# Performance work log

Measured on AMD Instinct MI355X. Metric: run time of the kernel, lower is better.

Reference implementation:

```python
import jax, jax.numpy as jnp
import numpy as np

B, S, HID = 2, 2048, 2048
H, KVH, D = 16, 4, 128
GROUPS = H // KVH  # 4


def apply_rotary(x, cos, sin):
    # x: [B, h, S, D]; cos/sin: [S, D//2]
    xr = x[..., 0::2]
    xi = x[..., 1::2]
    c = cos[None, None, :, :]
    s = sin[None, None, :, :]
    orr = xr * c - xi * s
    oi = xr * s + xi * c
    return jnp.stack([orr, oi], axis=-1).reshape(x.shape)


def setup_inputs() -> dict:
    key = jax.random.key(0)
    k0, k1, k2, k3, k4 = jax.random.split(key, 5)
    x = jax.random.normal(k0, (B, S, HID), dtype=jnp.float32)
    # real RoPE frequencies (llama-style), stored as [S, D//2, 2] = (cos, sin)
    inv_freq = 1.0 / (10000.0 ** (np.arange(0, D, 2, dtype=np.float32) / D))
    t = np.arange(S, dtype=np.float32)
    ang = np.outer(t, inv_freq)  # [S, D//2]
    freqs_cis = jnp.asarray(np.stack([np.cos(ang), np.sin(ang)], axis=-1), dtype=jnp.float32)
    sc = 0.02
    wq = jax.random.normal(k1, (HID, H * D), dtype=jnp.float32) * sc
    wk = jax.random.normal(k2, (HID, KVH * D), dtype=jnp.float32) * sc
    wv = jax.random.normal(k3, (HID, KVH * D), dtype=jnp.float32) * sc
    wo = jax.random.normal(k4, (H * D, HID), dtype=jnp.float32) * sc
    return {"x": x, "freqs_cis": freqs_cis, "wq": wq, "wk": wk, "wv": wv, "wo": wo}


def reference(x, freqs_cis, wq, wk, wv, wo):
    b, s, _ = x.shape
    cos, sin = freqs_cis[..., 0], freqs_cis[..., 1]
    q = (x @ wq).reshape(b, s, H, D).transpose(0, 2, 1, 3)    # [B,H,S,D]
    k = (x @ wk).reshape(b, s, KVH, D).transpose(0, 2, 1, 3)  # [B,KVH,S,D]
    v = (x @ wv).reshape(b, s, KVH, D).transpose(0, 2, 1, 3)
    q = apply_rotary(q, cos, sin)
    k = apply_rotary(k, cos, sin)
    # GQA expand: repeat kv heads into query-head groups
    k = jnp.repeat(k, GROUPS, axis=1)  # [B,H,S,D]
    v = jnp.repeat(v, GROUPS, axis=1)
    scale = 1.0 / jnp.sqrt(jnp.asarray(D, dtype=x.dtype))
    scores = jnp.einsum("bhqd,bhkd->bhqk", q, k) * scale
    causal = jnp.tril(jnp.ones((s, s), dtype=bool))
    scores = jnp.where(causal[None, None], scores, jnp.asarray(-jnp.inf, dtype=scores.dtype))
    attn = jax.nn.softmax(scores, axis=-1)
    out = jnp.einsum("bhqk,bhkd->bhqd", attn, v)
    out = out.transpose(0, 2, 1, 3).reshape(b, s, H * D)
    return out @ wo
```

## Files before the change

### kernel.cpp

```cpp
#include <hip/hip_runtime.h>
#include <hip/hip_bf16.h>

#define B_   2
#define S_   2048
#define HID_ 2048
#define H_   16
#define KVH_ 4
#define D_   128
#define M_   4096
#define NQKV 3072

typedef __attribute__((ext_vector_type(8))) short bf16x8;
typedef __attribute__((ext_vector_type(4))) float f32x4;
typedef const __attribute__((address_space(1))) unsigned int* gas_p;
typedef __attribute__((address_space(3))) unsigned int* las_p;

__device__ __forceinline__ unsigned short f2b(float f) {
    __hip_bfloat16 h = __float2bfloat16(f);
    return *reinterpret_cast<unsigned short*>(&h);
}
__device__ __forceinline__ float b2f(unsigned short u) {
    __hip_bfloat16 h;
    *reinterpret_cast<unsigned short*>(&h) = u;
    return __bfloat162float(h);
}

__global__ __launch_bounds__(256)
void convert_x(const float* __restrict__ x, unsigned short* __restrict__ xb) {
    int i = (blockIdx.x * 256 + threadIdx.x) * 4;
    float4 v = *(const float4*)(x + i);
    ushort4 o;
    o.x = f2b(v.x); o.y = f2b(v.y); o.z = f2b(v.z); o.w = f2b(v.w);
    *(ushort4*)(xb + i) = o;
}

__global__ __launch_bounds__(256)
void convert_w_all(const float* __restrict__ wq, const float* __restrict__ wk,
                   const float* __restrict__ wv, const float* __restrict__ wo,
                   unsigned short* __restrict__ wqkvT,
                   unsigned short* __restrict__ woT) {
    __shared__ float tile[32][33];
    int z = blockIdx.z;
    const float* w; int N, nbase; unsigned short* dst;
    if (z == 0)      { w = wq; N = 2048; nbase = 0;    dst = wqkvT; }
    else if (z == 1) { w = wk; N = 512;  nbase = 2048; dst = wqkvT; }
    else if (z == 2) { w = wv; N = 512;  nbase = 2560; dst = wqkvT; }
    else             { w = wo; N = 2048; nbase = 0;    dst = woT; }
    int n0 = blockIdx.x * 32, k0 = blockIdx.y * 32;
    if (n0 >= N) return;
    int tx = threadIdx.x & 31, ty = threadIdx.x >> 5;
    #pragma unroll
    for (int j = 0; j < 4; j++)
        tile[ty + j*8][tx] = w[(size_t)(k0 + ty + j*8) * N + n0 + tx];
    __syncthreads();
    #pragma unroll
    for (int j = 0; j < 4; j++)
        dst[(size_t)(nbase + n0 + ty + j*8) * 2048 + k0 + tx] = f2b(tile[tx][ty + j*8]);
}

#define BAR    asm volatile("s_barrier" ::: "memory")
#define LG0    do { asm volatile("s_waitcnt lgkmcnt(0)" ::: "memory"); \
                    __builtin_amdgcn_sched_barrier(0); } while (0)
#define GATE0  asm volatile("s_waitcnt vmcnt(0)" ::: "memory")
#define GATE6  asm volatile("s_waitcnt vmcnt(6)" ::: "memory")
#define GATE8  asm volatile("s_waitcnt vmcnt(8)" ::: "memory")
#define PHI    __builtin_amdgcn_s_setprio(1)
#define PLO    __builtin_amdgcn_s_setprio(0)

#define STG(srcrow, ldsbase, half, tile) do {                                   \
    _Pragma("unroll")                                                           \
    for (int it_ = 0; it_ < 2; ++it_) {                                         \
      int p_ = w * 128 + it_ * 64 + lane;                                       \
      int r_ = (half) * 128 + (p_ >> 3);                                        \
      int q8_ = ((p_ & 7) ^ ((p_ >> 3) & 7)) * 8;                               \
      __builtin_amdgcn_global_load_lds(                                         \
          (gas_p)((srcrow) + (size_t)r_ * 2048 + (tile) * 64 + q8_),            \
          (las_p)((char*)(ldsbase) + ((half) * 1024 + w * 128 + it_ * 64) * 16),\
          16, 0, 0);                                                            \
    } } while (0)

#define RDA2(dst, bufi, mi) do {                                                \
    const unsigned short* Ab_ = &As[bufi][0] + (mi)*8192 + wr*4096 + l15*64;    \
    _Pragma("unroll")                                                           \
    for (int f_ = 0; f_ < 4; ++f_) {                                            \
      dst[f_][0] = *(const bf16x8*)(Ab_ + f_*1024 + slot0);                     \
      dst[f_][1] = *(const bf16x8*)(Ab_ + f_*1024 + slot1);                     \
    } } while (0)

#define RDB2(dst, bufi, ni) do {                                                \
    const unsigned short* Bb_ = &Bs[bufi][0] + (ni)*8192 + wc*2048 + l15*64;    \
    _Pragma("unroll")                                                           \
    for (int g_ = 0; g_ < 2; ++g_) {                                            \
      dst[g_][0] = *(const bf16x8*)(Bb_ + g_*1024 + slot0);                     \
      dst[g_][1] = *(const bf16x8*)(Bb_ + g_*1024 + slot1);                     \
    } } while (0)

#define MMQ(ra, rb, mi, ni) do {                                                \
    _Pragma("unroll")                                                           \
    for (int f_ = 0; f_ < 4; ++f_)                                              \
      _Pragma("unroll")                                                         \
      for (int g_ = 0; g_ < 2; ++g_) {                                          \
        acc[(mi)*4+f_][(ni)*2+g_] = __builtin_amdgcn_mfma_f32_16x16x32_bf16(    \
            ra[f_][0], rb[g_][0], acc[(mi)*4+f_][(ni)*2+g_], 0, 0, 0);          \
        acc[(mi)*4+f_][(ni)*2+g_] = __builtin_amdgcn_mfma_f32_16x16x32_bf16(    \
            ra[f_][1], rb[g_][1], acc[(mi)*4+f_][(ni)*2+g_], 0, 0, 0);          \
      } } while (0)

__global__ __launch_bounds__(512)
void gemm8(const unsigned short* __restrict__ A,
           const unsigned short* __restrict__ BT,
           unsigned short* __restrict__ qkvb,
           unsigned short* __restrict__ vTb,
           const float* __restrict__ freqs) {
    __shared__ unsigned short As[2][16384];
    __shared__ unsigned short Bs[2][16384];

    int tid  = threadIdx.x;
    int lane = tid & 63, w = tid >> 6;
    int l15  = lane & 15, quad = lane >> 4;
    int wr = w >> 2, wc = w & 3;
    int bid = blockIdx.y * 12 + blockIdx.x;
    int s_  = (bid & 7) * 24 + (bid >> 3);
    int by  = s_ / 12, bx = s_ % 12;
    int row0 = by * 256, col0 = bx * 256;
    int slot0 = (quad ^ (lane & 7)) * 8;
    int slot1 = slot0 ^ 32;

    const unsigned short* Arow = A  + (size_t)row0 * 2048;
    const unsigned short* Brow = BT + (size_t)col0 * 2048;

    f32x4 acc[8][4];
    #pragma unroll
    for (int i = 0; i < 8; ++i)
        #pragma unroll
        for (int j = 0; j < 4; ++j) acc[i][j] = f32x4{0.f, 0.f, 0.f, 0.f};

    bf16x8 ra0[4][2], ra1[4][2];
    bf16x8 rb0[2][2], rb1[2][2];

    STG(Brow, &Bs[0][0], 0, 0);
    STG(Arow, &As[0][0], 0, 0);
    STG(Arow, &As[0][0], 1, 0);
    STG(Brow, &Bs[0][0], 1, 0);
    STG(Brow, &Bs[1][0], 0, 1);
    STG(Arow, &As[1][0], 0, 1);
    STG(Arow, &As[1][0], 1, 1);
    STG(Brow, &Bs[1][0], 1, 1);
    GATE8;
    BAR;
    RDB2(rb0, 0, 0);
    RDA2(ra0, 0, 0);

    #pragma unroll 1
    for (int i = 0; i < 16; ++i) {
        int t  = 2 * i;
        int t2 = (t + 2 > 31) ? 31 : t + 2;
        int t3 = (t + 3 > 31) ? 31 : t + 3;
        RDA2(ra1, 0, 1);
        STG(Brow, &Bs[0][0], 0, t2);
        PHI; MMQ(ra0, rb0, 0, 0); PLO;
        BAR;
        RDB2(rb1, 0, 1);
        STG(Arow, &As[0][0], 0, t2);
        PHI; MMQ(ra1, rb0, 1, 0); PLO;
        GATE8; BAR;
        RDB2(rb0, 1, 0);
        STG(Arow, &As[0][0], 1, t2);
        PHI; MMQ(ra0, rb1, 0, 1); PLO;
        BAR;
        RDA2(ra0, 1, 0);
        STG(Brow, &Bs[0][0], 1, t2);
        PHI; MMQ(ra1, rb1, 1, 1); PLO;
        GATE8; BAR;
        RDA2(ra1, 1, 1);
        STG(Brow, &Bs[1][0], 0, t3);
        PHI; MMQ(ra0, rb0, 0, 0); PLO;
        BAR;
        RDB2(rb1, 1, 1);
        STG(Arow, &As[1][0], 0, t3);
        PHI; MMQ(ra1, rb0, 1, 0); PLO;
        GATE8; BAR;
        RDB2(rb0, 0, 0);
        STG(Arow, &As[1][0], 1, t3);
        PHI; MMQ(ra0, rb1, 0, 1); PLO;
        BAR;
        RDA2(ra0, 0, 0);
        STG(Brow, &Bs[1][0], 1, t3);
        PHI; MMQ(ra1, rb1, 1, 1); PLO;
        GATE8; BAR;
    }

    int q4 = quad * 4;
    if (col0 < 2560) {
        const float qscale = 0.08838834764831845f;
        #pragma unroll
        for (int mi = 0; mi < 2; ++mi)
        #pragma unroll
        for (int f = 0; f < 4; ++f) {
            int mb = row0 + mi*128 + wr*64 + f*16 + q4;
            #pragma unroll
            for (int ni = 0; ni < 2; ++ni)
            #pragma unroll
            for (int g = 0; g < 2; ++g) {
                int colb = col0 + ni*128 + wc*32 + g*16 + l15;
                int dd = (colb & 127) & ~1;
                bool odd = colb & 1;
                float sc = (colb < 2048) ? qscale : 1.f;
                #pragma unroll
                for (int rr = 0; rr < 4; ++rr) {
                    int m = mb + rr;
                    int s = m & 2047;
                    float v  = acc[mi*4 + f][ni*2 + g][rr];
                    float pv = __shfl_xor(v, 1);
                    float cs = freqs[s*128 + dd];
                    float sn = freqs[s*128 + dd + 1];
                    float o  = odd ? (pv*sn + v*cs) : (v*cs - pv*sn);
                    qkvb[(size_t)m * NQKV + colb] = f2b(o * sc);
                }
            }
        }
    } else {
        #pragma unroll
        for (int mi = 0; mi < 2; ++mi)
        #pragma unroll
        for (int f = 0; f < 4; ++f) {
            int mb = row0 + mi*128 + wr*64 + f*16 + q4;
            int s0 = mb & 2047;
            #pragma unroll
            for (int ni = 0; ni < 2; ++ni)
            #pragma unroll
            for (int g = 0; g < 2; ++g) {
                int colb = col0 + ni*128 + wc*32 + g*16 + l15;
                int vrow = (row0 >> 11) * 512 + (colb - 2560);
                ushort4 ov;
                ov.x = f2b(acc[mi*4 + f][ni*2 + g][0]);
                ov.y = f2b(acc[mi*4 + f][ni*2 + g][1]);
                ov.z = f2b(acc[mi*4 + f][ni*2 + g][2]);
                ov.w = f2b(acc[mi*4 + f][ni*2 + g][3]);
                *(ushort4*)(vTb + (size_t)vrow * 2048 + s0) = ov;
            }
        }
    }
}

#define RDAo(bufi) do {                                                         \
    const unsigned short* Ab_ = &As[bufi][0] + wr * 4096 + l15 * 64;            \
    _Pragma("unroll")                                                           \
    for (int f_ = 0; f_ < 4; ++f_) {                                            \
      af[f_][0] = *(const bf16x8*)(Ab_ + f_ * 1024 + slot0);                    \
      af[f_][1] = *(const bf16x8*)(Ab_ + f_ * 1024 + slot1);                    \
    } } while (0)

#define RDBo(bufi, g) do {                                                      \
    const unsigned short* Bb_ = &Bs[bufi][0] + wc * 4096 + l15 * 64;            \
    bfr[g][0] = *(const bf16x8*)(Bb_ + (g) * 1024 + slot0);                     \
    bfr[g][1] = *(const bf16x8*)(Bb_ + (g) * 1024 + slot1);                     \
    } while (0)

#define MM8o(mi, ni) do {                                                       \
    _Pragma("unroll")                                                           \
    for (int f_ = 2*(mi); f_ < 2*(mi)+2; ++f_)                                  \
      _Pragma("unroll")                                                         \
      for (int g_ = 2*(ni); g_ < 2*(ni)+2; ++g_) {                              \
        acc[f_][g_] = __builtin_amdgcn_mfma_f32_16x16x32_bf16(                  \
            af[f_][0], bfr[g_][0], acc[f_][g_], 0, 0, 0);                       \
        acc[f_][g_] = __builtin_amdgcn_mfma_f32_16x16x32_bf16(                  \
            af[f_][1], bfr[g_][1], acc[f_][g_], 0, 0, 0);                       \
      } } while (0)

__global__ __launch_bounds__(512)
void gemm8o(const unsigned short* __restrict__ A,
            const unsigned short* __restrict__ BT,
            float* __restrict__ Cf) {
    __shared__ unsigned short As[2][16384];
    __shared__ unsigned short Bs[2][8192];

    int tid  = threadIdx.x;
    int lane = tid & 63, w = tid >> 6;
    int l15  = lane & 15, quad = lane >> 4;
    int wr = w >> 1, wc = w & 1;
    int bid = blockIdx.y * 16 + blockIdx.x;
    int s_  = (bid & 7) * 32 + (bid >> 3);
    int by  = s_ >> 4, bx = s_ & 15;
    int row0 = by * 256, col0 = bx * 128;
    int slot0 = (quad ^ (lane & 7)) * 8;
    int slot1 = slot0 ^ 32;

    const unsigned short* Arow = A  + (size_t)row0 * 2048;
    const unsigned short* Brow = BT + (size_t)col0 * 2048;

    f32x4 acc[4][4];
    #pragma unroll
    for (int i = 0; i < 4; ++i)
        #pragma unroll
        for (int j = 0; j < 4; ++j) acc[i][j] = f32x4{0.f, 0.f, 0.f, 0.f};

    bf16x8 af[4][2];
    bf16x8 bfr[4][2];

    STG(Arow, &As[0][0], 0, 0);
    STG(Arow, &As[0][0], 1, 0);
    STG(Brow, &Bs[0][0], 0, 0);
    STG(Arow, &As[1][0], 0, 1);
    STG(Arow, &As[1][0], 1, 1);
    STG(Brow, &Bs[1][0], 0, 1);
    GATE6;
    BAR;

    #pragma unroll 1
    for (int i = 0; i < 15; ++i) {
        int t = 2 * i;
        RDAo(0); RDBo(0, 0); RDBo(0, 1);
        BAR; LG0; PHI; MM8o(0, 0); PLO; BAR;
        RDBo(0, 2); RDBo(0, 3); STG(Arow, &As[0][0], 0, t + 2);
        BAR; LG0; PHI; MM8o(0, 1); PLO; BAR;
        STG(Arow, &As[0][0], 1, t + 2);
        BAR; LG0; PHI; MM8o(1, 0); PLO; BAR;
        STG(Brow, &Bs[0][0], 0, t + 2);
        BAR; LG0; PHI; MM8o(1, 1); PLO; GATE6; BAR;
        RDAo(1); RDBo(1, 0); RDBo(1, 1);
        BAR; LG0; PHI; MM8o(0, 0); PLO; BAR;
        RDBo(1, 2); RDBo(1, 3); STG(Arow, &As[1][0], 0, t + 3);
        BAR; LG0; PHI; MM8o(0, 1); PLO; BAR;
        STG(Arow, &As[1][0], 1, t + 3);
        BAR; LG0; PHI; MM8o(1, 0); PLO; BAR;
        STG(Brow, &Bs[1][0], 0, t + 3);
        BAR; LG0; PHI; MM8o(1, 1); PLO; GATE6; BAR;
    }
    RDAo(0); RDBo(0, 0); RDBo(0, 1);
    BAR; LG0; PHI; MM8o(0, 0); PLO; BAR;
    RDBo(0, 2); RDBo(0, 3);
    BAR; LG0; PHI; MM8o(0, 1); PLO; BAR;
    BAR; LG0; PHI; MM8o(1, 0); PLO; BAR;
    BAR; LG0; PHI; MM8o(1, 1); PLO; GATE0; BAR;
    RDAo(1); RDBo(1, 0); RDBo(1, 1);
    BAR; LG0; PHI; MM8o(0, 0); PLO; BAR;
    RDBo(1, 2); RDBo(1, 3);
    BAR; LG0; PHI; MM8o(0, 1); PLO; BAR;
    BAR; LG0; PHI; MM8o(1, 0); PLO; BAR;
    LG0; PHI; MM8o(1, 1); PLO;

    int q4 = quad * 4;
    #pragma unroll
    for (int f = 0; f < 4; ++f) {
        int mb = row0 + wr*64 + f*16 + q4;
        #pragma unroll
        for (int g = 0; g < 4; ++g) {
            int colb = col0 + wc*64 + g*16 + l15;
            #pragma unroll
            for (int rr = 0; rr < 4; ++rr)
                Cf[(size_t)(mb + rr) * 2048 + colb] = acc[f][g][rr];
        }
    }
}

__global__ __launch_bounds__(512)
void attn_mfma(const unsigned short* __restrict__ qkv,
               const unsigned short* __restrict__ vT,
               unsigned short* __restrict__ ao,
               unsigned short* __restrict__ wsP,
               float2* __restrict__ wsML) {
    __shared__ unsigned short Ks[64 * 128];
    __shared__ unsigned short Vt[128 * 64];

    int tid  = threadIdx.x;
    int lane = tid & 63, w = tid >> 6;
    int quad = lane >> 4, l15 = lane & 15;
    int hw = w >> 1, qhalf = w & 1;
    int bx = blockIdx.x, hk = blockIdx.y, b = blockIdx.z;
    int h = hk * 4 + hw;

    int qt, c;
    if (bx < 12)      { qt = 31 - bx / 3;        c = bx % 3; }
    else if (bx < 40) { qt = 27 - (bx - 12) / 2; c = (bx - 12) & 1; }
    else              { qt = 53 - bx;            c = 0; }
    int nt = qt + 1;
    int nch = (qt >= 28) ? 3 : (qt >= 14 ? 2 : 1);
    int kt_begin = c * 14;
    int kt_end = (nt < (c + 1) * 14) ? nt : (c + 1) * 14;
    bool lastc = (c == nch - 1);
    int q0 = qt * 64;

    bf16x8 aq[2][4];
    #pragma unroll
    for (int qf = 0; qf < 2; qf++) {
        const unsigned short* qrow =
            qkv + (size_t)(b*2048 + q0 + qhalf*32 + qf*16 + l15) * NQKV + h*128;
        #pragma unroll
        for (int k4 = 0; k4 < 4; k4++)
            aq[qf][k4] = *(const bf16x8*)(qrow + k4*32 + quad*8);
    }

    int koff[4][4];
    #pragma unroll
    for (int j = 0; j < 4; j++) {
        int row = ((j >> 1) * 32) + ((l15 >> 2) * 8) + ((j & 1) * 4) + (l15 & 3);
        #pragma unroll
        for (int k4 = 0; k4 < 4; k4++) {
            int slot = (k4 * 4 + quad) ^ (row & 15);
            koff[j][k4] = (row * 16 + slot) * 8;
        }
    }
    int vbase0 = (l15 * 8 + (quad ^ (l15 & 7))) * 8;
    int vbase1 = (l15 * 8 + ((4 + quad) ^ (l15 & 7))) * 8;

    const unsigned short* kb0 = qkv + (size_t)(b*2048) * NQKV + 2048 + hk*128;
    const unsigned short* vb0 = vT + (size_t)(b*512 + hk*128) * 2048;

    auto stage_k = [&](int kt) {
        #pragma unroll
        for (int it = 0; it < 2; it++) {
            int s = w * 128 + it * 64 + lane;
            int r = s >> 4, qp = s & 15;
            int q = qp ^ (r & 15);
            __builtin_amdgcn_global_load_lds(
                (gas_p)(kb0 + (size_t)(kt*64 + r) * NQKV + q * 8),
                (las_p)((char*)&Ks[0] + (w * 128 + it * 64) * 16),
                16, 0, 0);
        }
    };
    auto stage_v = [&](int kt) {
        #pragma unroll
        for (int it = 0; it < 2; it++) {
            int s = w * 128 + it * 64 + lane;
            int r = s >> 3, qp = s & 7;
            int q = qp ^ (r & 7);
            __builtin_amdgcn_global_load_lds(
                (gas_p)(vb0 + (size_t)r * 2048 + kt*64 + q * 8),
                (las_p)((char*)&Vt[0] + (w * 128 + it * 64) * 16),
                16, 0, 0);
        }
    };

    f32x4 o_acc[2][8];
    const f32x4 zf = {0.f, 0.f, 0.f, 0.f};
    #pragma unroll
    for (int qf = 0; qf < 2; qf++)
        #pragma unroll
        for (int jn = 0; jn < 8; jn++) o_acc[qf][jn] = zf;
    float m_i[2] = {-1e30f, -1e30f}, l_i[2] = {0.f, 0.f};
    int qglob[2] = {q0 + qhalf*32 + l15, q0 + qhalf*32 + 16 + l15};

    stage_k(kt_begin);
    for (int kt = kt_begin; kt < kt_end; kt++) {
        __syncthreads();
        stage_v(kt);

        f32x4 s_acc[2][4];
        #pragma unroll
        for (int j = 0; j < 4; j++) {
            s_acc[0][j] = zf; s_acc[1][j] = zf;
            #pragma unroll
            for (int k4 = 0; k4 < 4; k4++) {
                bf16x8 ak = *(const bf16x8*)&Ks[koff[j][k4]];
                s_acc[0][j] = __builtin_amdgcn_mfma_f32_16x16x32_bf16(ak, aq[0][k4], s_acc[0][j], 0, 0, 0);
                s_acc[1][j] = __builtin_amdgcn_mfma_f32_16x16x32_bf16(ak, aq[1][k4], s_acc[1][j], 0, 0, 0);
            }
        }

        bf16x8 pp[2][2];
        #pragma unroll
        for (int qf = 0; qf < 2; qf++) {
            float sv[4][4];
            #pragma unroll
            for (int j = 0; j < 4; j++)
                #pragma unroll
                for (int r = 0; r < 4; r++)
                    sv[j][r] = s_acc[qf][j][r];
            if (kt == qt) {
                #pragma unroll
                for (int j = 0; j < 4; j++)
                    #pragma unroll
                    for (int r = 0; r < 4; r++) {
                        int sloc = ((j >> 1) * 32) + quad*8 + ((j & 1) * 4) + r;
                        if (kt*64 + sloc > qglob[qf]) sv[j][r] = -1e30f;
                    }
            }
            float mx = sv[0][0];
            #pragma unroll
            for (int j = 0; j < 4; j++)
                #pragma unroll
                for (int r = 0; r < 4; r++) mx = fmaxf(mx, sv[j][r]);
            mx = fmaxf(mx, __shfl_xor(mx, 16));
            mx = fmaxf(mx, __shfl_xor(mx, 32));
            int defer = __all(mx <= m_i[qf] + 8.f);
            float mnew = defer ? m_i[qf] : fmaxf(m_i[qf], mx);
            float rs = 0.f;
            float p[4][4];
            #pragma unroll
            for (int j = 0; j < 4; j++)
                #pragma unroll
                for (int r = 0; r < 4; r++) {
                    p[j][r] = __expf(sv[j][r] - mnew);
                    rs += p[j][r];
                }
            if (!defer) {
                float alpha = __expf(m_i[qf] - mnew);
                l_i[qf] *= alpha;
                #pragma unroll
                for (int jn = 0; jn < 8; jn++)
                    #pragma unroll
                    for (int r = 0; r < 4; r++) o_acc[qf][jn][r] *= alpha;
                m_i[qf] = mnew;
            }
            l_i[qf] += rs;
            #pragma unroll
            for (int r = 0; r < 4; r++) {
                pp[qf][0][r]     = (short)f2b(p[0][r]);
                pp[qf][0][r + 4] = (short)f2b(p[1][r]);
                pp[qf][1][r]     = (short)f2b(p[2][r]);
                pp[qf][1][r + 4] = (short)f2b(p[3][r]);
            }
        }

        __syncthreads();
        if (kt + 1 < kt_end) stage_k(kt + 1);

        #pragma unroll
        for (int jn = 0; jn < 8; jn++) {
            bf16x8 av0 = *(const bf16x8*)&Vt[jn*1024 + vbase0];
            bf16x8 av1 = *(const bf16x8*)&Vt[jn*1024 + vbase1];
            o_acc[0][jn] = __builtin_amdgcn_mfma_f32_16x16x32_bf16(av0, pp[0][0], o_acc[0][jn], 0, 0, 0);
            o_acc[0][jn] = __builtin_amdgcn_mfma_f32_16x16x32_bf16(av1, pp[0][1], o_acc[0][jn], 0, 0, 0);
            o_acc[1][jn] = __builtin_amdgcn_mfma_f32_16x16x32_bf16(av0, pp[1][0], o_acc[1][jn], 0, 0, 0);
            o_acc[1][jn] = __builtin_amdgcn_mfma_f32_16x16x32_bf16(av1, pp[1][1], o_acc[1][jn], 0, 0, 0);
        }
    }

    int pi = 0, mi = 0;
    if (qt >= 14) {
        if (qt < 28) { mi = (qt - 14) * 2 + c;       pi = qt - 14; }
        else         { mi = 28 + (qt - 28) * 3 + c;  pi = 14 + (qt - 28) * 2 + c; }
    }
    #pragma unroll
    for (int qf = 0; qf < 2; qf++) {
        float lt = l_i[qf];
        lt += __shfl_xor(lt, 16);
        lt += __shfl_xor(lt, 32);
        float inv = 1.f / lt;
        int q_local = qhalf * 32 + qf * 16 + l15;
        unsigned short* dst;
        if (lastc)
            dst = ao + (size_t)(b*2048 + q0 + q_local) * 2048 + h*128;
        else
            dst = wsP + (size_t)(((pi * 8 + hk * 2 + b) * 4 + hw) * 64 + q_local) * 128;
        #pragma unroll
        for (int jn = 0; jn < 8; jn++) {
            ushort4 ov;
            ov.x = f2b(o_acc[qf][jn][0] * inv);
            ov.y = f2b(o_acc[qf][jn][1] * inv);
            ov.z = f2b(o_acc[qf][jn][2] * inv);
            ov.w = f2b(o_acc[qf][jn][3] * inv);
            *(ushort4*)(dst + jn*16 + quad*4) = ov;
        }
        if (qt >= 14 && quad == 0)
            wsML[(mi * 8 + hk * 2 + b) * 256 + hw * 64 + q_local]
                = make_float2(m_i[qf], lt);
    }
}

__global__ __launch_bounds__(256)
void merge_kernel(unsigned short* __restrict__ ao,
                  const unsigned short* __restrict__ wsP,
                  const float2* __restrict__ wsML) {
    int t = blockIdx.x * 256 + threadIdx.x;
    int d = (t & 15) * 8;
    int h = (t >> 4) & 15;
    int rest = t >> 8;
    int q_off = rest % 1152;
    int b = rest / 1152;
    int q = 896 + q_off;
    int qt = q >> 6, q_local = q & 63;
    int hk = h >> 2, hw = h & 3;
    int nch = (qt >= 28) ? 3 : 2;

    float mv[3], lv[3];
    for (int cc = 0; cc < nch; cc++) {
        int mi = (qt < 28) ? (qt - 14) * 2 + cc : 28 + (qt - 28) * 3 + cc;
        float2 ml = wsML[(mi * 8 + hk * 2 + b) * 256 + hw * 64 + q_local];
        mv[cc] = ml.x; lv[cc] = ml.y;
    }
    float M = mv[0];
    for (int cc = 1; cc < nch; cc++) M = fmaxf(M, mv[cc]);
    float f[3], S = 0.f;
    for (int cc = 0; cc < nch; cc++) { f[cc] = __expf(mv[cc] - M) * lv[cc]; S += f[cc]; }
    float inv = 1.f / S;

    unsigned short* arow = ao + (size_t)(b*2048 + q) * 2048 + h*128 + d;
    float outv[8];
    {
        ushort4 a0 = *(ushort4*)arow, a1 = *(ushort4*)(arow + 4);
        float fl = f[nch-1];
        outv[0] = fl*b2f(a0.x); outv[1] = fl*b2f(a0.y);
        outv[2] = fl*b2f(a0.z); outv[3] = fl*b2f(a0.w);
        outv[4] = fl*b2f(a1.x); outv[5] = fl*b2f(a1.y);
        outv[6] = fl*b2f(a1.z); outv[7] = fl*b2f(a1.w);
    }
    for (int cc = 0; cc < nch - 1; cc++) {
        int pi = (qt < 28) ? (qt - 14) : 14 + (qt - 28) * 2 + cc;
        const unsigned short* prow =
            wsP + (size_t)(((pi * 8 + hk * 2 + b) * 4 + hw) * 64 + q_local) * 128 + d;
        ushort4 p0 = *(const ushort4*)prow, p1 = *(const ushort4*)(prow + 4);
        float fc = f[cc];
        outv[0] += fc*b2f(p0.x); outv[1] += fc*b2f(p0.y);
        outv[2] += fc*b2f(p0.z); outv[3] += fc*b2f(p0.w);
        outv[4] += fc*b2f(p1.x); outv[5] += fc*b2f(p1.y);
        outv[6] += fc*b2f(p1.z); outv[7] += fc*b2f(p1.w);
    }
    ushort4 o0, o1;
    o0.x = f2b(outv[0]*inv); o0.y = f2b(outv[1]*inv);
    o0.z = f2b(outv[2]*inv); o0.w = f2b(outv[3]*inv);
    o1.x = f2b(outv[4]*inv); o1.y = f2b(outv[5]*inv);
    o1.z = f2b(outv[6]*inv); o1.w = f2b(outv[7]*inv);
    *(ushort4*)arow = o0;
    *(ushort4*)(arow + 4) = o1;
}

extern "C" void kernel_launch(void* const* d_in, const int* in_sizes, int n_in,
                              void* d_out, int out_size, void* d_ws, size_t ws_size,
                              hipStream_t stream) {
    const float* x     = (const float*)d_in[0];
    const float* freqs = (const float*)d_in[1];
    const float* wq    = (const float*)d_in[2];
    const float* wk    = (const float*)d_in[3];
    const float* wv    = (const float*)d_in[4];
    const float* wo    = (const float*)d_in[5];
    float* out = (float*)d_out;

    char* ws = (char*)d_ws;
    unsigned short* xbf    = (unsigned short*)(ws);
    unsigned short* aobuf  = (unsigned short*)(ws);
    unsigned short* wqkvT  = (unsigned short*)(ws + (16u<<20));
    unsigned short* woT    = (unsigned short*)(ws + (28u<<20));
    unsigned short* qkvbuf = (unsigned short*)(ws + (36u<<20));
    unsigned short* vTbuf  = (unsigned short*)(ws + (60u<<20));
    unsigned short* wsP  = (unsigned short*)(ws + (16u<<20));
    float2*         wsML = (float2*)(ws + (16u<<20) + 176u*65536u);

    dim3 blk(256);
    convert_x<<<8192, blk, 0, stream>>>(x, xbf);
    convert_w_all<<<dim3(64, 64, 4), blk, 0, stream>>>(wq, wk, wv, wo, wqkvT, woT);
    gemm8<<<dim3(NQKV/256, M_/256), dim3(512), 0, stream>>>(
        xbf, wqkvT, qkvbuf, vTbuf, freqs);
    attn_mfma<<<dim3(54, 4, 2), dim3(512), 0, stream>>>(qkvbuf, vTbuf, aobuf, wsP, wsML);
    merge_kernel<<<2304, blk, 0, stream>>>(aobuf, wsP, wsML);
    gemm8o<<<dim3(2048/128, M_/256), dim3(512), 0, stream>>>(aobuf, woT, out);
}
```

Before: 319.3 us.

## Retile QKV GEMM to 256x192 tiles and merge conversion kernels

The QKV projection GEMM moves from 256x256 tiles on a 12x16 grid to 256x192 tiles on a 16x16 grid. This gives 256 workgroups, matching the CU count better and removing the partial last wave. The warp layout changes from 2x4 to 4x2 and the main loop is restructured with finer barrier and lgkmcnt gating plus a peeled epilogue. The Q/K/V epilogue branch becomes per-column-group because a tile now straddles regions. The x and weight conversion kernels are fused into one launch to save a kernel launch, at the cost of more barriers per K step in the GEMM.

```diff
diff --git a/kernel.cpp b/kernel.cpp
--- a/kernel.cpp
+++ b/kernel.cpp
@@ -26,21 +26,23 @@
 }
 
 __global__ __launch_bounds__(256)
-void convert_x(const float* __restrict__ x, unsigned short* __restrict__ xb) {
-    int i = (blockIdx.x * 256 + threadIdx.x) * 4;
-    float4 v = *(const float4*)(x + i);
-    ushort4 o;
-    o.x = f2b(v.x); o.y = f2b(v.y); o.z = f2b(v.z); o.w = f2b(v.w);
-    *(ushort4*)(xb + i) = o;
-}
-
-__global__ __launch_bounds__(256)
-void convert_w_all(const float* __restrict__ wq, const float* __restrict__ wk,
-                   const float* __restrict__ wv, const float* __restrict__ wo,
-                   unsigned short* __restrict__ wqkvT,
-                   unsigned short* __restrict__ woT) {
+void convert_all(const float* __restrict__ x,
+                 const float* __restrict__ wq, const float* __restrict__ wk,
+                 const float* __restrict__ wv, const float* __restrict__ wo,
+                 unsigned short* __restrict__ xb,
+                 unsigned short* __restrict__ wqkvT,
+                 unsigned short* __restrict__ woT) {
+    int z = blockIdx.z;
+    if (z >= 4) {
+        int lin = ((z - 4) * 64 + blockIdx.y) * 64 + blockIdx.x;
+        int i = (lin * 256 + threadIdx.x) * 4;
+        float4 v = *(const float4*)(x + i);
+        ushort4 o;
+        o.x = f2b(v.x); o.y = f2b(v.y); o.z = f2b(v.z); o.w = f2b(v.w);
+        *(ushort4*)(xb + i) = o;
+        return;
+    }
     __shared__ float tile[32][33];
-    int z = blockIdx.z;
     const float* w; int N, nbase; unsigned short* dst;
     if (z == 0)      { w = wq; N = 2048; nbase = 0;    dst = wqkvT; }
     else if (z == 1) { w = wk; N = 512;  nbase = 2048; dst = wqkvT; }
@@ -63,7 +65,7 @@
                     __builtin_amdgcn_sched_barrier(0); } while (0)
 #define GATE0  asm volatile("s_waitcnt vmcnt(0)" ::: "memory")
 #define GATE6  asm volatile("s_waitcnt vmcnt(6)" ::: "memory")
-#define GATE8  asm volatile("s_waitcnt vmcnt(8)" ::: "memory")
+#define GATE7  asm volatile("s_waitcnt vmcnt(7)" ::: "memory")
 #define PHI    __builtin_amdgcn_s_setprio(1)
 #define PLO    __builtin_amdgcn_s_setprio(0)
 
@@ -79,31 +81,41 @@
           16, 0, 0);                                                            \
     } } while (0)
 
-#define RDA2(dst, bufi, mi) do {                                                \
-    const unsigned short* Ab_ = &As[bufi][0] + (mi)*8192 + wr*4096 + l15*64;    \
+#define STGB(srcrow, ldsbase, unit, tile) do {                                  \
+      int p_ = w * 64 + lane;                                                   \
+      int r_ = (unit) * 64 + (p_ >> 3);                                         \
+      int q8_ = ((p_ & 7) ^ ((p_ >> 3) & 7)) * 8;                               \
+      __builtin_amdgcn_global_load_lds(                                         \
+          (gas_p)((srcrow) + (size_t)r_ * 2048 + (tile) * 64 + q8_),            \
+          (las_p)((char*)(ldsbase) + ((unit) * 512 + p_) * 16),                 \
+          16, 0, 0);                                                            \
+    } while (0)
+
+#define RDAq(dst, bufi) do {                                                    \
+    const unsigned short* Ab_ = &As[bufi][0] + wr*4096 + l15*64;                \
     _Pragma("unroll")                                                           \
     for (int f_ = 0; f_ < 4; ++f_) {                                            \
       dst[f_][0] = *(const bf16x8*)(Ab_ + f_*1024 + slot0);                     \
       dst[f_][1] = *(const bf16x8*)(Ab_ + f_*1024 + slot1);                     \
     } } while (0)
 
-#define RDB2(dst, bufi, ni) do {                                                \
-    const unsigned short* Bb_ = &Bs[bufi][0] + (ni)*8192 + wc*2048 + l15*64;    \
+#define RDBq(dst, bufi, nh) do {                                                \
+    const unsigned short* Bb_ = &Bs[bufi][0] + wc*6144 + (nh)*3072 + l15*64;    \
     _Pragma("unroll")                                                           \
-    for (int g_ = 0; g_ < 2; ++g_) {                                            \
+    for (int g_ = 0; g_ < 3; ++g_) {                                            \
       dst[g_][0] = *(const bf16x8*)(Bb_ + g_*1024 + slot0);                     \
       dst[g_][1] = *(const bf16x8*)(Bb_ + g_*1024 + slot1);                     \
     } } while (0)
 
-#define MMQ(ra, rb, mi, ni) do {                                                \
+#define MMq(mh, rb, nh) do {                                                    \
     _Pragma("unroll")                                                           \
-    for (int f_ = 0; f_ < 4; ++f_)                                              \
+    for (int f_ = 2*(mh); f_ < 2*(mh)+2; ++f_)                                  \
       _Pragma("unroll")                                                         \
-      for (int g_ = 0; g_ < 2; ++g_) {                                          \
-        acc[(mi)*4+f_][(ni)*2+g_] = __builtin_amdgcn_mfma_f32_16x16x32_bf16(    \
-            ra[f_][0], rb[g_][0], acc[(mi)*4+f_][(ni)*2+g_], 0, 0, 0);          \
-        acc[(mi)*4+f_][(ni)*2+g_] = __builtin_amdgcn_mfma_f32_16x16x32_bf16(    \
-            ra[f_][1], rb[g_][1], acc[(mi)*4+f_][(ni)*2+g_], 0, 0, 0);          \
+      for (int g_ = 0; g_ < 3; ++g_) {                                          \
+        acc[f_][(nh)*3+g_] = __builtin_amdgcn_mfma_f32_16x16x32_bf16(           \
+            ra[f_][0], rb[g_][0], acc[f_][(nh)*3+g_], 0, 0, 0);                 \
+        acc[f_][(nh)*3+g_] = __builtin_amdgcn_mfma_f32_16x16x32_bf16(           \
+            ra[f_][1], rb[g_][1], acc[f_][(nh)*3+g_], 0, 0, 0);                 \
       } } while (0)
 
 __global__ __launch_bounds__(512)
@@ -113,130 +125,114 @@
            unsigned short* __restrict__ vTb,
            const float* __restrict__ freqs) {
     __shared__ unsigned short As[2][16384];
-    __shared__ unsigned short Bs[2][16384];
+    __shared__ unsigned short Bs[2][12288];
 
     int tid  = threadIdx.x;
     int lane = tid & 63, w = tid >> 6;
     int l15  = lane & 15, quad = lane >> 4;
-    int wr = w >> 2, wc = w & 3;
-    int bid = blockIdx.y * 12 + blockIdx.x;
-    int s_  = (bid & 7) * 24 + (bid >> 3);
-    int by  = s_ / 12, bx = s_ % 12;
-    int row0 = by * 256, col0 = bx * 256;
+    int wr = w >> 1, wc = w & 1;
+    int bid = blockIdx.y * 16 + blockIdx.x;
+    int s_  = (bid & 7) * 32 + (bid >> 3);
+    int by  = s_ >> 4, bx = s_ & 15;
+    int row0 = by * 256, col0 = bx * 192;
     int slot0 = (quad ^ (lane & 7)) * 8;
     int slot1 = slot0 ^ 32;
 
     const unsigned short* Arow = A  + (size_t)row0 * 2048;
     const unsigned short* Brow = BT + (size_t)col0 * 2048;
 
-    f32x4 acc[8][4];
-    #pragma unroll
-    for (int i = 0; i < 8; ++i)
-        #pragma unroll
-        for (int j = 0; j < 4; ++j) acc[i][j] = f32x4{0.f, 0.f, 0.f, 0.f};
-
-    bf16x8 ra0[4][2], ra1[4][2];
-    bf16x8 rb0[2][2], rb1[2][2];
-
-    STG(Brow, &Bs[0][0], 0, 0);
-    STG(Arow, &As[0][0], 0, 0);
-    STG(Arow, &As[0][0], 1, 0);
-    STG(Brow, &Bs[0][0], 1, 0);
-    STG(Brow, &Bs[1][0], 0, 1);
-    STG(Arow, &As[1][0], 0, 1);
-    STG(Arow, &As[1][0], 1, 1);
-    STG(Brow, &Bs[1][0], 1, 1);
-    GATE8;
+    f32x4 acc[4][6];
+    #pragma unroll
+    for (int i = 0; i < 4; ++i)
+        #pragma unroll
+        for (int j = 0; j < 6; ++j) acc[i][j] = f32x4{0.f, 0.f, 0.f, 0.f};
+
+    bf16x8 ra[4][2];
+    bf16x8 rbl[3][2];
+    bf16x8 rbh[3][2];
+
+    STG (Arow, &As[0][0], 0, 0);
+    STG (Arow, &As[0][0], 1, 0);
+    STGB(Brow, &Bs[0][0], 0, 0);
+    STGB(Brow, &Bs[0][0], 1, 0);
+    STGB(Brow, &Bs[0][0], 2, 0);
+    STG (Arow, &As[1][0], 0, 1);
+    STG (Arow, &As[1][0], 1, 1);
+    STGB(Brow, &Bs[1][0], 0, 1);
+    STGB(Brow, &Bs[1][0], 1, 1);
+    STGB(Brow, &Bs[1][0], 2, 1);
+    GATE7;
     BAR;
-    RDB2(rb0, 0, 0);
-    RDA2(ra0, 0, 0);
 
     #pragma unroll 1
-    for (int i = 0; i < 16; ++i) {
-        int t  = 2 * i;
-        int t2 = (t + 2 > 31) ? 31 : t + 2;
-        int t3 = (t + 3 > 31) ? 31 : t + 3;
-        RDA2(ra1, 0, 1);
-        STG(Brow, &Bs[0][0], 0, t2);
-        PHI; MMQ(ra0, rb0, 0, 0); PLO;
-        BAR;
-        RDB2(rb1, 0, 1);
-        STG(Arow, &As[0][0], 0, t2);
-        PHI; MMQ(ra1, rb0, 1, 0); PLO;
-        GATE8; BAR;
-        RDB2(rb0, 1, 0);
-        STG(Arow, &As[0][0], 1, t2);
-        PHI; MMQ(ra0, rb1, 0, 1); PLO;
-        BAR;
-        RDA2(ra0, 1, 0);
-        STG(Brow, &Bs[0][0], 1, t2);
-        PHI; MMQ(ra1, rb1, 1, 1); PLO;
-        GATE8; BAR;
-        RDA2(ra1, 1, 1);
-        STG(Brow, &Bs[1][0], 0, t3);
-        PHI; MMQ(ra0, rb0, 0, 0); PLO;
-        BAR;
-        RDB2(rb1, 1, 1);
-        STG(Arow, &As[1][0], 0, t3);
-        PHI; MMQ(ra1, rb0, 1, 0); PLO;
-        GATE8; BAR;
-        RDB2(rb0, 0, 0);
-        STG(Arow, &As[1][0], 1, t3);
-        PHI; MMQ(ra0, rb1, 0, 1); PLO;
-        BAR;
-        RDA2(ra0, 0, 0);
-        STG(Brow, &Bs[1][0], 1, t3);
-        PHI; MMQ(ra1, rb1, 1, 1); PLO;
-        GATE8; BAR;
-    }
+    for (int i = 0; i < 15; ++i) {
+        int t = 2 * i;
+        RDAq(ra, 0); RDBq(rbl, 0, 0);
+        BAR; LG0; PHI; MMq(0, rbl, 0); PLO; BAR;
+        RDBq(rbh, 0, 1); STG(Arow, &As[0][0], 0, t + 2);
+        BAR; LG0; PHI; MMq(0, rbh, 1); PLO; BAR;
+        STG(Arow, &As[0][0], 1, t + 2);
+        BAR; LG0; PHI; MMq(1, rbl, 0); PLO; BAR;
+        STGB(Brow, &Bs[0][0], 0, t + 2);
+        STGB(Brow, &Bs[0][0], 1, t + 2);
+        STGB(Brow, &Bs[0][0], 2, t + 2);
+        BAR; LG0; PHI; MMq(1, rbh, 1); PLO; GATE7; BAR;
+        RDAq(ra, 1); RDBq(rbl, 1, 0);
+        BAR; LG0; PHI; MMq(0, rbl, 0); PLO; BAR;
+        RDBq(rbh, 1, 1); STG(Arow, &As[1][0], 0, t + 3);
+        BAR; LG0; PHI; MMq(0, rbh, 1); PLO; BAR;
+        STG(Arow, &As[1][0], 1, t + 3);
+        BAR; LG0; PHI; MMq(1, rbl, 0); PLO; BAR;
+        STGB(Brow, &Bs[1][0], 0, t + 3);
+        STGB(Brow, &Bs[1][0], 1, t + 3);
+        STGB(Brow, &Bs[1][0], 2, t + 3);
+        BAR; LG0; PHI; MMq(1, rbh, 1); PLO; GATE7; BAR;
+    }
+    RDAq(ra, 0); RDBq(rbl, 0, 0);
+    BAR; LG0; PHI; MMq(0, rbl, 0); PLO; BAR;
+    RDBq(rbh, 0, 1);
+    BAR; LG0; PHI; MMq(0, rbh, 1); PLO; BAR;
+    BAR; LG0; PHI; MMq(1, rbl, 0); PLO; BAR;
+    BAR; LG0; PHI; MMq(1, rbh, 1); PLO; GATE0; BAR;
+    RDAq(ra, 1); RDBq(rbl, 1, 0);
+    BAR; LG0; PHI; MMq(0, rbl, 0); PLO; BAR;
+    RDBq(rbh, 1, 1);
+    BAR; LG0; PHI; MMq(0, rbh, 1); PLO; BAR;
+    BAR; LG0; PHI; MMq(1, rbl, 0); PLO; BAR;
+    LG0; PHI; MMq(1, rbh, 1); PLO;
 
     int q4 = quad * 4;
-    if (col0 < 2560) {
-        const float qscale = 0.08838834764831845f;
-        #pragma unroll
-        for (int mi = 0; mi < 2; ++mi)
-        #pragma unroll
-        for (int f = 0; f < 4; ++f) {
-            int mb = row0 + mi*128 + wr*64 + f*16 + q4;
-            #pragma unroll
-            for (int ni = 0; ni < 2; ++ni)
-            #pragma unroll
-            for (int g = 0; g < 2; ++g) {
-                int colb = col0 + ni*128 + wc*32 + g*16 + l15;
+    const float qscale = 0.08838834764831845f;
+    #pragma unroll
+    for (int f = 0; f < 4; ++f) {
+        int mb = row0 + wr*64 + f*16 + q4;
+        #pragma unroll
+        for (int g = 0; g < 6; ++g) {
+            int colbase = col0 + wc*96 + g*16;
+            int colb = colbase + l15;
+            if (colbase < 2560) {
                 int dd = (colb & 127) & ~1;
                 bool odd = colb & 1;
-                float sc = (colb < 2048) ? qscale : 1.f;
+                float sc = (colbase < 2048) ? qscale : 1.f;
                 #pragma unroll
                 for (int rr = 0; rr < 4; ++rr) {
                     int m = mb + rr;
                     int s = m & 2047;
-                    float v  = acc[mi*4 + f][ni*2 + g][rr];
+                    float v  = acc[f][g][rr];
                     float pv = __shfl_xor(v, 1);
                     float cs = freqs[s*128 + dd];
                     float sn = freqs[s*128 + dd + 1];
                     float o  = odd ? (pv*sn + v*cs) : (v*cs - pv*sn);
                     qkvb[(size_t)m * NQKV + colb] = f2b(o * sc);
                 }
-            }
-        }
-    } else {
-        #pragma unroll
-        for (int mi = 0; mi < 2; ++mi)
-        #pragma unroll
-        for (int f = 0; f < 4; ++f) {
-            int mb = row0 + mi*128 + wr*64 + f*16 + q4;
-            int s0 = mb & 2047;
-            #pragma unroll
-            for (int ni = 0; ni < 2; ++ni)
-            #pragma unroll
-            for (int g = 0; g < 2; ++g) {
-                int colb = col0 + ni*128 + wc*32 + g*16 + l15;
+            } else {
                 int vrow = (row0 >> 11) * 512 + (colb - 2560);
+                int s0 = mb & 2047;
                 ushort4 ov;
-                ov.x = f2b(acc[mi*4 + f][ni*2 + g][0]);
-                ov.y = f2b(acc[mi*4 + f][ni*2 + g][1]);
-                ov.z = f2b(acc[mi*4 + f][ni*2 + g][2]);
-                ov.w = f2b(acc[mi*4 + f][ni*2 + g][3]);
+                ov.x = f2b(acc[f][g][0]);
+                ov.y = f2b(acc[f][g][1]);
+                ov.z = f2b(acc[f][g][2]);
+                ov.w = f2b(acc[f][g][3]);
                 *(ushort4*)(vTb + (size_t)vrow * 2048 + s0) = ov;
             }
         }
@@ -637,12 +633,11 @@
     unsigned short* wsP  = (unsigned short*)(ws + (16u<<20));
     float2*         wsML = (float2*)(ws + (16u<<20) + 176u*65536u);
 
-    dim3 blk(256);
-    convert_x<<<8192, blk, 0, stream>>>(x, xbf);
-    convert_w_all<<<dim3(64, 64, 4), blk, 0, stream>>>(wq, wk, wv, wo, wqkvT, woT);
-    gemm8<<<dim3(NQKV/256, M_/256), dim3(512), 0, stream>>>(
+    convert_all<<<dim3(64, 64, 6), dim3(256), 0, stream>>>(
+        x, wq, wk, wv, wo, xbf, wqkvT, woT);
+    gemm8<<<dim3(16, 16), dim3(512), 0, stream>>>(
         xbf, wqkvT, qkvbuf, vTbuf, freqs);
     attn_mfma<<<dim3(54, 4, 2), dim3(512), 0, stream>>>(qkvbuf, vTbuf, aobuf, wsP, wsML);
-    merge_kernel<<<2304, blk, 0, stream>>>(aobuf, wsP, wsML);
+    merge_kernel<<<2304, dim3(256), 0, stream>>>(aobuf, wsP, wsML);
     gemm8o<<<dim3(2048/128, M_/256), dim3(512), 0, stream>>>(aobuf, woT, out);
 }
```

Measured after the change: 293.4 us. 8.1% less time.
